# Kernel optimization log

Hardware: AMD Instinct MI355X
Metric: run time of the kernel (lower is better)

## Reference

```python
import jax, jax.numpy as jnp
import numpy as np

NUM_HEADS = 8
HEAD_CH = 32  # embed_channels // num_heads = 256 // 8
BN_EPS = 1e-3


def _conv(x, w, pad):
    return jax.lax.conv_general_dilated(
        x, w, window_strides=(1, 1), padding=[(pad, pad), (pad, pad)],
        dimension_numbers=('NCHW', 'OIHW', 'NCHW'))


def _bn(x, gamma, beta):
    # inference BN with running_mean=0, running_var=1 (fresh buffers)
    scale = gamma / jnp.sqrt(1.0 + BN_EPS)
    return x * scale[None, :, None, None] + beta[None, :, None, None]


def setup_inputs() -> dict:
    key = jax.random.key(0)
    ks = jax.random.split(key, 8)
    B, Cin, H, W = 16, 512, 40, 40
    N, Cg, E, Cout = 80, 512, 256, 512
    s = 0.05
    return {
        'x': jax.random.normal(ks[0], (B, Cin, H, W), jnp.float32),
        'guide': jax.random.normal(ks[1], (B, N, Cg), jnp.float32),
        'We': jax.random.normal(ks[2], (E, Cin, 1, 1), jnp.float32) * s,
        'gamma_e': jnp.ones((E,), jnp.float32),
        'beta_e': jnp.zeros((E,), jnp.float32),
        'Wg': jax.random.normal(ks[3], (E, Cg), jnp.float32) * s,
        'bg': jnp.zeros((E,), jnp.float32),
        'head_bias': jnp.zeros((NUM_HEADS,), jnp.float32),
        'Wp': jax.random.normal(ks[4], (Cout, Cin, 3, 3), jnp.float32) * s,
        'gamma_p': jnp.ones((Cout,), jnp.float32),
        'beta_p': jnp.zeros((Cout,), jnp.float32),
    }


def reference(x, guide, We, gamma_e, beta_e, Wg, bg, head_bias, Wp, gamma_p, beta_p):
    B, _, H, W = x.shape
    M, C = NUM_HEADS, HEAD_CH
    # guide_fc: [B, n, Cg] -> [B, n, M, C]
    g = (jnp.einsum('bnc,ec->bne', guide, Wg) + bg).reshape(B, -1, M, C)
    # embed_conv (1x1 + BN, no act): [B, M, C, H, W]
    e = _bn(_conv(x, We, 0), gamma_e, beta_e).reshape(B, M, C, H, W)
    # attention scores, max over guide tokens, scale, bias, sigmoid
    attn = jnp.einsum('bmchw,bnmc->bmhwn', e, g)
    attn = jnp.max(attn, axis=-1) / (C ** 0.5)
    attn = jax.nn.sigmoid(attn + head_bias[None, :, None, None])
    # project_conv (3x3 + BN, no act), gated per head
    p = _bn(_conv(x, Wp, 1), gamma_p, beta_p)
    p = p.reshape(B, M, -1, H, W) * attn[:, :, None, :, :]
    return p.reshape(B, -1, H, W)
```

## Files before the change

kernel.cpp:

```cpp
#include <hip/hip_runtime.h>
#include <hip/hip_bf16.h>
#include <stdint.h>

#define B_   16
#define CIN  512
#define HW   1600
#define E_   256
#define NTOK 80
#define CG   512
#define COUT 512
#define NHEAD 8
#define HCH  32
#define SP   (42*42)

typedef __attribute__((ext_vector_type(8))) short bf16x8;
typedef __attribute__((ext_vector_type(4))) float f32x4;
typedef unsigned short ushort_t;

__device__ __forceinline__ unsigned short f2bf(float f) {
  union { float f; unsigned int i; } v; v.f = f;
  unsigned int x = v.i;
  return (unsigned short)((x + 0x7FFFu + ((x >> 16) & 1u)) >> 16);
}

__global__ void k_prep_x(const float* __restrict__ x, unsigned short* __restrict__ xt) {
  __shared__ float tile[32][33];
  int hw0 = blockIdx.x * 32, ci0 = blockIdx.y * 32, b = blockIdx.z;
  int tx = threadIdx.x, ty = threadIdx.y;
  const float* xp = x + ((size_t)b * CIN + ci0) * HW + hw0;
#pragma unroll
  for (int j = 0; j < 4; j++) tile[ty + 8 * j][tx] = xp[(size_t)(ty + 8 * j) * HW + tx];
  __syncthreads();
  int ci = ci0 + tx;
#pragma unroll
  for (int j = 0; j < 4; j++) {
    int hw = hw0 + ty + 8 * j;
    int h = hw / 40, w = hw - h * 40;
    xt[((size_t)b * SP + (size_t)(h + 1) * 42 + (w + 1)) * CIN + ci] = f2bf(tile[tx][ty + 8 * j]);
  }
}

__global__ void k_prep_wp(const float* __restrict__ Wp, unsigned short* __restrict__ wpb2) {
  int idx = blockIdx.x * 256 + threadIdx.x;
  int co = idx >> 9, ci = idx & 511;
  const float* s = Wp + (size_t)idx * 9;
#pragma unroll
  for (int t = 0; t < 9; t++) wpb2[(size_t)co * (9 * CIN) + t * CIN + ci] = f2bf(s[t]);
}

__global__ void k_cast4(const float* __restrict__ in, unsigned short* __restrict__ out, int n4) {
  int i = blockIdx.x * 256 + threadIdx.x;
  if (i < n4) {
    float4 v = ((const float4*)in)[i];
    ushort4 o; o.x = f2bf(v.x); o.y = f2bf(v.y); o.z = f2bf(v.z); o.w = f2bf(v.w);
    ((ushort4*)out)[i] = o;
  }
}

template<int NTAPS, int EPI, int MT, int NT, int NB>
__launch_bounds__(256)
__global__ void k_conv(const unsigned short* __restrict__ Aw,
                       const unsigned short* __restrict__ Bsrc,
                       const float* __restrict__ gamma, const float* __restrict__ beta,
                       const float* __restrict__ attn, float* __restrict__ outp,
                       unsigned short* __restrict__ et, int Ncols) {
  constexpr int  RS    = NTAPS * CIN;
  constexpr int  NSTEP = NTAPS * (CIN / 32);
  constexpr bool BLIN  = (EPI == 2);
  __shared__ unsigned short L[3 * 8192];
  char* LB = (char*)L;
  int tid = threadIdx.x;

  int wg = blockIdx.x;
  if constexpr ((MT * NT * NB) % 8 == 0 && NB > 1) {
    constexpr int q = (MT * NT * NB) / 8;
    wg = (wg & 7) * q + (wg >> 3);
  }
  constexpr int PB = MT * NT;
  int b = wg / PB;
  int rem = wg - b * PB;
  int ntile = rem % NT;
  int mtile = rem / NT;
  int m0 = mtile * 128, n0 = ntile * 128;

  int lane = tid & 63, wid = tid >> 6;
  int wr = wid >> 1, wc = wid & 1;

  int mA = tid >> 2;
  int kq_log = (tid & 3) ^ ((tid >> 3) & 3);
  int kg = kq_log * 8;
  unsigned int lds0 = (unsigned int)tid * 16u, lds1 = (unsigned int)tid * 16u + 4096u;

  const unsigned short* pA = Aw + (size_t)(m0 + mA) * RS + kg;
  const unsigned short* pB0;
  const unsigned short* pB1;
  if constexpr (BLIN) {
    pB0 = Bsrc + (size_t)(n0 + mA) * CIN + kg;
    pB1 = Bsrc + (size_t)(n0 + mA + 64) * CIN + kg;
  } else {
    int hw_a = n0 + mA;      if (hw_a > HW - 1) hw_a = HW - 1;
    int hw_b = n0 + mA + 64; if (hw_b > HW - 1) hw_b = HW - 1;
    int ha = hw_a / 40, wa = hw_a - ha * 40;
    int hb = hw_b / 40, wb = hw_b - hb * 40;
    int sp_a = ha * 42 + wa + ((NTAPS == 1) ? 43 : 0);
    int sp_b = hb * 42 + wb + ((NTAPS == 1) ? 43 : 0);
    const unsigned short* xtb = Bsrc + (size_t)b * SP * CIN;
    pB0 = xtb + (size_t)sp_a * CIN + kg;
    pB1 = xtb + (size_t)sp_b * CIN + kg;
  }

  int scnt = 0;
  auto STG = [&](unsigned bo) {
    __builtin_amdgcn_global_load_lds((const __attribute__((address_space(1))) unsigned int*)pA,
        (__attribute__((address_space(3))) unsigned int*)(LB + bo + lds0), 16, 0, 0);
    __builtin_amdgcn_global_load_lds((const __attribute__((address_space(1))) unsigned int*)(pA + 64 * RS),
        (__attribute__((address_space(3))) unsigned int*)(LB + bo + lds1), 16, 0, 0);
    __builtin_amdgcn_global_load_lds((const __attribute__((address_space(1))) unsigned int*)pB0,
        (__attribute__((address_space(3))) unsigned int*)(LB + bo + 8192u + lds0), 16, 0, 0);
    __builtin_amdgcn_global_load_lds((const __attribute__((address_space(1))) unsigned int*)pB1,
        (__attribute__((address_space(3))) unsigned int*)(LB + bo + 8192u + lds1), 16, 0, 0);
    pA += 32; pB0 += 32; pB1 += 32;
    if constexpr (NTAPS > 1) {
      ++scnt;
      if ((scnt % 48) == 0) { pB0 += 19968; pB1 += 19968; }
    }
  };

  int frow = lane & 15;
  int kq16 = lane >> 4;
  int swz = (kq16 ^ ((frow >> 1) & 3)) << 4;
  int aoff[4], boff[4];
#pragma unroll
  for (int i = 0; i < 4; i++) {
    aoff[i] = (wr * 64 + i * 16 + frow) * 64 + swz;
    boff[i] = 8192 + (wc * 64 + i * 16 + frow) * 64 + swz;
  }

  f32x4 acc[4][4] = {};

  STG(0u); STG(16384u);
  unsigned r0 = 0u, r1 = 16384u, r2 = 32768u;
  for (int s = 0; s < NSTEP; ++s) {
    if (s + 1 < NSTEP) { asm volatile("s_waitcnt vmcnt(4)" ::: "memory"); }
    else               { asm volatile("s_waitcnt vmcnt(0)" ::: "memory"); }
    __builtin_amdgcn_s_barrier();
    __builtin_amdgcn_sched_barrier(0);
    if (s + 2 < NSTEP) STG(r2);
    const char* base = LB + r0;
    bf16x8 af[4], bfv[4];
#pragma unroll
    for (int i = 0; i < 4; i++) af[i] = *(const bf16x8*)(base + aoff[i]);
#pragma unroll
    for (int i = 0; i < 4; i++) bfv[i] = *(const bf16x8*)(base + boff[i]);
#pragma unroll
    for (int mi = 0; mi < 4; mi++)
#pragma unroll
      for (int ni = 0; ni < 4; ni++)
        acc[mi][ni] = __builtin_amdgcn_mfma_f32_16x16x32_bf16(af[mi], bfv[ni], acc[mi][ni], 0, 0, 0);
    unsigned t = r0; r0 = r1; r1 = r2; r2 = t;
  }

  const float BN_RSQ = 0.9995003746877732f;
  int colb = n0 + wc * 64 + frow;
  int rowb = m0 + wr * 64 + (lane >> 4) * 4;
  if constexpr (EPI == 1) {
    int head = (m0 + wr * 64) >> 6;
    const float* attn_b = attn + ((size_t)b * NHEAD + head) * HW;
    float* ob = outp + (size_t)b * COUT * HW;
#pragma unroll
    for (int mi = 0; mi < 4; mi++) {
      float sc[4], bt[4];
#pragma unroll
      for (int j = 0; j < 4; j++) {
        int co = rowb + mi * 16 + j;
        sc[j] = gamma[co] * BN_RSQ; bt[j] = beta[co];
      }
#pragma unroll
      for (int ni = 0; ni < 4; ni++) {
        int hw = colb + ni * 16;
        if (hw < Ncols) {
          float gate = attn_b[hw];
#pragma unroll
          for (int j = 0; j < 4; j++) {
            int co = rowb + mi * 16 + j;
            ob[(size_t)co * HW + hw] = (acc[mi][ni][j] * sc[j] + bt[j]) * gate;
          }
        }
      }
    }
  } else {
    unsigned short* etb = et + (EPI == 0 ? (size_t)b * HW * E_ : (size_t)0);
#pragma unroll
    for (int mi = 0; mi < 4; mi++) {
      float sc[4], bt[4];
#pragma unroll
      for (int j = 0; j < 4; j++) {
        int ech = rowb + mi * 16 + j;
        sc[j] = (EPI == 2) ? 1.0f : gamma[ech] * BN_RSQ;
        bt[j] = beta[ech];
      }
#pragma unroll
      for (int ni = 0; ni < 4; ni++) {
        int hw = colb + ni * 16;
        if (hw < Ncols) {
          ushort4 pk;
          pk.x = f2bf(acc[mi][ni][0] * sc[0] + bt[0]);
          pk.y = f2bf(acc[mi][ni][1] * sc[1] + bt[1]);
          pk.z = f2bf(acc[mi][ni][2] * sc[2] + bt[2]);
          pk.w = f2bf(acc[mi][ni][3] * sc[3] + bt[3]);
          *(ushort4*)(etb + (size_t)hw * E_ + (rowb + mi * 16)) = pk;
        }
      }
    }
  }
}

__global__ void k_attn_mfma(const unsigned short* __restrict__ et, const unsigned short* __restrict__ gbf,
                            const float* __restrict__ head_bias, float* __restrict__ attn) {
  __shared__ unsigned short gs[NTOK * HCH];
  int b = blockIdx.z, m = blockIdx.y;
  int tid = threadIdx.x, lane = tid & 63, wid = tid >> 6;
  for (int i = tid; i < NTOK * HCH / 8; i += 256) {
    int n = i >> 2, c = (i & 3) * 8;
    *(bf16x8*)&gs[n * HCH + c] = *(const bf16x8*)&gbf[((size_t)b * NTOK + n) * E_ + m * HCH + c];
  }
  __syncthreads();
  int col = lane & 15, kq = (lane >> 4) * 8;
  bf16x8 bfr[5];
#pragma unroll
  for (int ni = 0; ni < 5; ni++)
    bfr[ni] = *(const bf16x8*)&gs[(ni * 16 + col) * HCH + kq];

  int hw0 = blockIdx.x * 256 + wid * 64;
  bf16x8 afr[4];
#pragma unroll
  for (int mi = 0; mi < 4; mi++) {
    int hw = hw0 + mi * 16 + col; if (hw > HW - 1) hw = HW - 1;
    afr[mi] = *(const bf16x8*)&et[((size_t)b * HW + hw) * E_ + m * HCH + kq];
  }
  float hb = head_bias[m];
  float* attnp = attn + ((size_t)b * NHEAD + m) * HW;
#pragma unroll
  for (int mi = 0; mi < 4; mi++) {
    f32x4 d[5];
#pragma unroll
    for (int ni = 0; ni < 5; ni++) {
      f32x4 z = {0.f, 0.f, 0.f, 0.f};
      d[ni] = __builtin_amdgcn_mfma_f32_16x16x32_bf16(afr[mi], bfr[ni], z, 0, 0, 0);
    }
#pragma unroll
    for (int j = 0; j < 4; j++) {
      float v = fmaxf(fmaxf(fmaxf(d[0][j], d[1][j]), fmaxf(d[2][j], d[3][j])), d[4][j]);
      v = fmaxf(v, __shfl_xor(v, 1, 16));
      v = fmaxf(v, __shfl_xor(v, 2, 16));
      v = fmaxf(v, __shfl_xor(v, 4, 16));
      v = fmaxf(v, __shfl_xor(v, 8, 16));
      if (col == j) {
        int hwout = hw0 + mi * 16 + (lane >> 4) * 4 + j;
        if (hwout < HW)
          attnp[hwout] = 1.0f / (1.0f + __expf(-(v * 0.17677669529663687f + hb)));
      }
    }
  }
}

extern "C" void kernel_launch(void* const* d_in, const int* in_sizes, int n_in,
                              void* d_out, int out_size, void* d_ws, size_t ws_size,
                              hipStream_t stream) {
  const float* x         = (const float*)d_in[0];
  const float* guide     = (const float*)d_in[1];
  const float* We        = (const float*)d_in[2];
  const float* gamma_e   = (const float*)d_in[3];
  const float* beta_e    = (const float*)d_in[4];
  const float* Wg        = (const float*)d_in[5];
  const float* bg        = (const float*)d_in[6];
  const float* head_bias = (const float*)d_in[7];
  const float* Wp        = (const float*)d_in[8];
  const float* gamma_p   = (const float*)d_in[9];
  const float* beta_p    = (const float*)d_in[10];
  float* out = (float*)d_out;

  char* ws = (char*)d_ws;
  size_t off = 0;
  auto alloc = [&](size_t bytes) { char* p = ws + off; off += (bytes + 255) & ~(size_t)255; return p; };
  unsigned short* xt   = (unsigned short*)alloc((size_t)B_ * SP * CIN * 2);
  unsigned short* wpb2 = (unsigned short*)alloc((size_t)COUT * 9 * CIN * 2);
  unsigned short* web  = (unsigned short*)alloc((size_t)E_ * CIN * 2);
  unsigned short* wgb  = (unsigned short*)alloc((size_t)E_ * CG * 2);
  unsigned short* gub  = (unsigned short*)alloc((size_t)B_ * NTOK * CG * 2);
  unsigned short* gbf  = (unsigned short*)alloc((size_t)B_ * NTOK * E_ * 2);
  unsigned short* et   = (unsigned short*)alloc((size_t)B_ * HW * E_ * 2);
  float* attn          = (float*)alloc((size_t)B_ * NHEAD * HW * 4);

  hipMemsetAsync(xt, 0, (size_t)B_ * SP * CIN * 2, stream);
  k_prep_x<<<dim3(50, 16, B_), dim3(32, 8), 0, stream>>>(x, xt);
  k_prep_wp<<<dim3(1024), dim3(256), 0, stream>>>(Wp, wpb2);
  k_cast4<<<dim3(128), dim3(256), 0, stream>>>(We, web, E_ * CIN / 4);
  k_cast4<<<dim3(128), dim3(256), 0, stream>>>(Wg, wgb, E_ * CG / 4);
  k_cast4<<<dim3(640), dim3(256), 0, stream>>>(guide, gub, B_ * NTOK * CG / 4);
  k_conv<1, 2, 2, 10, 1><<<dim3(20), dim3(256), 0, stream>>>(wgb, gub, bg, bg, nullptr, nullptr, gbf, B_ * NTOK);
  k_conv<1, 0, 2, 13, B_><<<dim3(2 * 13 * B_), dim3(256), 0, stream>>>(web, xt, gamma_e, beta_e, nullptr, nullptr, et, HW);
  k_attn_mfma<<<dim3(7, NHEAD, B_), dim3(256), 0, stream>>>(et, gbf, head_bias, attn);
  k_conv<9, 1, 4, 13, B_><<<dim3(4 * 13 * B_), dim3(256), 0, stream>>>(wpb2, xt, gamma_p, beta_p, attn, out, nullptr, HW);
}
```

Measured before the change: 327.1 us.

## Enlarge GEMM tiles to 256x128 and flatten batch into column dimension

```diff
diff --git a/kernel.cpp b/kernel.cpp
--- a/kernel.cpp
+++ b/kernel.cpp
@@ -15,7 +15,6 @@
 
 typedef __attribute__((ext_vector_type(8))) short bf16x8;
 typedef __attribute__((ext_vector_type(4))) float f32x4;
-typedef unsigned short ushort_t;
 
 __device__ __forceinline__ unsigned short f2bf(float f) {
   union { float f; unsigned int i; } v; v.f = f;
@@ -48,77 +47,74 @@
   for (int t = 0; t < 9; t++) wpb2[(size_t)co * (9 * CIN) + t * CIN + ci] = f2bf(s[t]);
 }
 
-__global__ void k_cast4(const float* __restrict__ in, unsigned short* __restrict__ out, int n4) {
+__global__ void k_cast_all(const float* __restrict__ We, unsigned short* __restrict__ web,
+                           const float* __restrict__ Wg, unsigned short* __restrict__ wgb,
+                           const float* __restrict__ gu, unsigned short* __restrict__ gub) {
   int i = blockIdx.x * 256 + threadIdx.x;
-  if (i < n4) {
-    float4 v = ((const float4*)in)[i];
-    ushort4 o; o.x = f2bf(v.x); o.y = f2bf(v.y); o.z = f2bf(v.z); o.w = f2bf(v.w);
-    ((ushort4*)out)[i] = o;
-  }
-}
-
-template<int NTAPS, int EPI, int MT, int NT, int NB>
-__launch_bounds__(256)
+  const float* src; unsigned short* dst; int j;
+  if (i < 32768)       { src = We; dst = web; j = i; }
+  else if (i < 65536)  { src = Wg; dst = wgb; j = i - 32768; }
+  else                 { src = gu; dst = gub; j = i - 65536; }
+  float4 v = ((const float4*)src)[j];
+  ushort4 o; o.x = f2bf(v.x); o.y = f2bf(v.y); o.z = f2bf(v.z); o.w = f2bf(v.w);
+  ((ushort4*)dst)[j] = o;
+}
+
+template<int NTAPS, int EPI, int MT, int NT, int SWZ>
+__launch_bounds__(256, 2)
 __global__ void k_conv(const unsigned short* __restrict__ Aw,
                        const unsigned short* __restrict__ Bsrc,
                        const float* __restrict__ gamma, const float* __restrict__ beta,
                        const float* __restrict__ attn, float* __restrict__ outp,
-                       unsigned short* __restrict__ et, int Ncols) {
+                       unsigned short* __restrict__ et) {
   constexpr int  RS    = NTAPS * CIN;
   constexpr int  NSTEP = NTAPS * (CIN / 32);
   constexpr bool BLIN  = (EPI == 2);
-  __shared__ unsigned short L[3 * 8192];
+  __shared__ unsigned short L[3 * 12288];
   char* LB = (char*)L;
   int tid = threadIdx.x;
 
   int wg = blockIdx.x;
-  if constexpr ((MT * NT * NB) % 8 == 0 && NB > 1) {
-    constexpr int q = (MT * NT * NB) / 8;
+  if constexpr (SWZ) {
+    constexpr int q = MT * NT / 8;
     wg = (wg & 7) * q + (wg >> 3);
   }
-  constexpr int PB = MT * NT;
-  int b = wg / PB;
-  int rem = wg - b * PB;
-  int ntile = rem % NT;
-  int mtile = rem / NT;
-  int m0 = mtile * 128, n0 = ntile * 128;
+  int mtile = wg / NT, ntile = wg % NT;
+  int m0 = mtile * 256, n0 = ntile * 128;
 
   int lane = tid & 63, wid = tid >> 6;
   int wr = wid >> 1, wc = wid & 1;
 
-  int mA = tid >> 2;
-  int kq_log = (tid & 3) ^ ((tid >> 3) & 3);
-  int kg = kq_log * 8;
-  unsigned int lds0 = (unsigned int)tid * 16u, lds1 = (unsigned int)tid * 16u + 4096u;
-
-  const unsigned short* pA = Aw + (size_t)(m0 + mA) * RS + kg;
+  int rA = tid >> 2;
+  int kq = ((tid & 3) ^ ((tid >> 3) & 3)) * 8;
+  const unsigned short* pA = Aw + (size_t)(m0 + rA) * RS + kq;
   const unsigned short* pB0;
   const unsigned short* pB1;
   if constexpr (BLIN) {
-    pB0 = Bsrc + (size_t)(n0 + mA) * CIN + kg;
-    pB1 = Bsrc + (size_t)(n0 + mA + 64) * CIN + kg;
+    pB0 = Bsrc + (size_t)(n0 + rA) * CIN + kq;
+    pB1 = pB0 + (size_t)64 * CIN;
   } else {
-    int hw_a = n0 + mA;      if (hw_a > HW - 1) hw_a = HW - 1;
-    int hw_b = n0 + mA + 64; if (hw_b > HW - 1) hw_b = HW - 1;
-    int ha = hw_a / 40, wa = hw_a - ha * 40;
-    int hb = hw_b / 40, wb = hw_b - hb * 40;
-    int sp_a = ha * 42 + wa + ((NTAPS == 1) ? 43 : 0);
-    int sp_b = hb * 42 + wb + ((NTAPS == 1) ? 43 : 0);
-    const unsigned short* xtb = Bsrc + (size_t)b * SP * CIN;
-    pB0 = xtb + (size_t)sp_a * CIN + kg;
-    pB1 = xtb + (size_t)sp_b * CIN + kg;
+    int c0 = n0 + rA, c1 = c0 + 64;
+    int b0 = c0 / 1600, hw0 = c0 - b0 * 1600;
+    int b1 = c1 / 1600, hw1 = c1 - b1 * 1600;
+    int h0 = hw0 / 40, w0 = hw0 - h0 * 40;
+    int h1 = hw1 / 40, w1 = hw1 - h1 * 40;
+    constexpr int ctr = (NTAPS == 1) ? 43 : 0;
+    pB0 = Bsrc + ((size_t)b0 * SP + h0 * 42 + w0 + ctr) * CIN + kq;
+    pB1 = Bsrc + ((size_t)b1 * SP + h1 * 42 + w1 + ctr) * CIN + kq;
   }
 
   int scnt = 0;
   auto STG = [&](unsigned bo) {
-    __builtin_amdgcn_global_load_lds((const __attribute__((address_space(1))) unsigned int*)pA,
-        (__attribute__((address_space(3))) unsigned int*)(LB + bo + lds0), 16, 0, 0);
-    __builtin_amdgcn_global_load_lds((const __attribute__((address_space(1))) unsigned int*)(pA + 64 * RS),
-        (__attribute__((address_space(3))) unsigned int*)(LB + bo + lds1), 16, 0, 0);
-    __builtin_amdgcn_global_load_lds((const __attribute__((address_space(1))) unsigned int*)pB0,
-        (__attribute__((address_space(3))) unsigned int*)(LB + bo + 8192u + lds0), 16, 0, 0);
-    __builtin_amdgcn_global_load_lds((const __attribute__((address_space(1))) unsigned int*)pB1,
-        (__attribute__((address_space(3))) unsigned int*)(LB + bo + 8192u + lds1), 16, 0, 0);
+#define GL(src, dst) __builtin_amdgcn_global_load_lds((const __attribute__((address_space(1))) unsigned int*)(src), \
+        (__attribute__((address_space(3))) unsigned int*)(dst), 16, 0, 0)
+    GL(pA,            LB + bo +      0u + tid * 16u);
+    GL(pA +  64 * RS, LB + bo +  4096u + tid * 16u);
+    GL(pA + 128 * RS, LB + bo +  8192u + tid * 16u);
+    GL(pA + 192 * RS, LB + bo + 12288u + tid * 16u);
+    GL(pB0,           LB + bo + 16384u + tid * 16u);
+    GL(pB1,           LB + bo + 20480u + tid * 16u);
+#undef GL
     pA += 32; pB0 += 32; pB1 += 32;
     if constexpr (NTAPS > 1) {
       ++scnt;
@@ -127,48 +123,45 @@
   };
 
   int frow = lane & 15;
-  int kq16 = lane >> 4;
-  int swz = (kq16 ^ ((frow >> 1) & 3)) << 4;
-  int aoff[4], boff[4];
-#pragma unroll
-  for (int i = 0; i < 4; i++) {
-    aoff[i] = (wr * 64 + i * 16 + frow) * 64 + swz;
-    boff[i] = 8192 + (wc * 64 + i * 16 + frow) * 64 + swz;
-  }
-
-  f32x4 acc[4][4] = {};
-
-  STG(0u); STG(16384u);
-  unsigned r0 = 0u, r1 = 16384u, r2 = 32768u;
+  int swz = ((lane >> 4) ^ ((frow >> 1) & 3)) << 4;
+  int aoff[8], boff[4];
+#pragma unroll
+  for (int i = 0; i < 8; i++) aoff[i] = (wr * 128 + i * 16 + frow) * 64 + swz;
+#pragma unroll
+  for (int i = 0; i < 4; i++) boff[i] = 16384 + (wc * 64 + i * 16 + frow) * 64 + swz;
+
+  f32x4 acc[8][4] = {};
+
+  STG(0u); STG(24576u);
+  unsigned r0 = 0u, r1 = 24576u, r2 = 49152u;
   for (int s = 0; s < NSTEP; ++s) {
-    if (s + 1 < NSTEP) { asm volatile("s_waitcnt vmcnt(4)" ::: "memory"); }
+    if (s + 1 < NSTEP) { asm volatile("s_waitcnt vmcnt(6)" ::: "memory"); }
     else               { asm volatile("s_waitcnt vmcnt(0)" ::: "memory"); }
     __builtin_amdgcn_s_barrier();
     __builtin_amdgcn_sched_barrier(0);
     if (s + 2 < NSTEP) STG(r2);
     const char* base = LB + r0;
-    bf16x8 af[4], bfv[4];
-#pragma unroll
-    for (int i = 0; i < 4; i++) af[i] = *(const bf16x8*)(base + aoff[i]);
-#pragma unroll
-    for (int i = 0; i < 4; i++) bfv[i] = *(const bf16x8*)(base + boff[i]);
-#pragma unroll
-    for (int mi = 0; mi < 4; mi++)
+    bf16x8 af[8], bv[4];
+#pragma unroll
+    for (int i = 0; i < 8; i++) af[i] = *(const bf16x8*)(base + aoff[i]);
+#pragma unroll
+    for (int i = 0; i < 4; i++) bv[i] = *(const bf16x8*)(base + boff[i]);
+#pragma unroll
+    for (int mi = 0; mi < 8; mi++)
 #pragma unroll
       for (int ni = 0; ni < 4; ni++)
-        acc[mi][ni] = __builtin_amdgcn_mfma_f32_16x16x32_bf16(af[mi], bfv[ni], acc[mi][ni], 0, 0, 0);
+        acc[mi][ni] = __builtin_amdgcn_mfma_f32_16x16x32_bf16(af[mi], bv[ni], acc[mi][ni], 0, 0, 0);
     unsigned t = r0; r0 = r1; r1 = r2; r2 = t;
   }
 
   const float BN_RSQ = 0.9995003746877732f;
   int colb = n0 + wc * 64 + frow;
-  int rowb = m0 + wr * 64 + (lane >> 4) * 4;
+  int rowb = m0 + wr * 128 + (lane >> 4) * 4;
   if constexpr (EPI == 1) {
-    int head = (m0 + wr * 64) >> 6;
-    const float* attn_b = attn + ((size_t)b * NHEAD + head) * HW;
-    float* ob = outp + (size_t)b * COUT * HW;
-#pragma unroll
-    for (int mi = 0; mi < 4; mi++) {
+    float* ob = outp;
+#pragma unroll
+    for (int mi = 0; mi < 8; mi++) {
+      int head = (m0 + wr * 128 + mi * 16) >> 6;
       float sc[4], bt[4];
 #pragma unroll
       for (int j = 0; j < 4; j++) {
@@ -177,21 +170,19 @@
       }
 #pragma unroll
       for (int ni = 0; ni < 4; ni++) {
-        int hw = colb + ni * 16;
-        if (hw < Ncols) {
-          float gate = attn_b[hw];
-#pragma unroll
-          for (int j = 0; j < 4; j++) {
-            int co = rowb + mi * 16 + j;
-            ob[(size_t)co * HW + hw] = (acc[mi][ni][j] * sc[j] + bt[j]) * gate;
-          }
+        int col = colb + ni * 16;
+        int b = col / 1600, hw = col - b * 1600;
+        float gate = attn[((size_t)b * NHEAD + head) * HW + hw];
+#pragma unroll
+        for (int j = 0; j < 4; j++) {
+          int co = rowb + mi * 16 + j;
+          ob[((size_t)b * COUT + co) * HW + hw] = (acc[mi][ni][j] * sc[j] + bt[j]) * gate;
         }
       }
     }
   } else {
-    unsigned short* etb = et + (EPI == 0 ? (size_t)b * HW * E_ : (size_t)0);
-#pragma unroll
-    for (int mi = 0; mi < 4; mi++) {
+#pragma unroll
+    for (int mi = 0; mi < 8; mi++) {
       float sc[4], bt[4];
 #pragma unroll
       for (int j = 0; j < 4; j++) {
@@ -201,15 +192,20 @@
       }
 #pragma unroll
       for (int ni = 0; ni < 4; ni++) {
-        int hw = colb + ni * 16;
-        if (hw < Ncols) {
-          ushort4 pk;
-          pk.x = f2bf(acc[mi][ni][0] * sc[0] + bt[0]);
-          pk.y = f2bf(acc[mi][ni][1] * sc[1] + bt[1]);
-          pk.z = f2bf(acc[mi][ni][2] * sc[2] + bt[2]);
-          pk.w = f2bf(acc[mi][ni][3] * sc[3] + bt[3]);
-          *(ushort4*)(etb + (size_t)hw * E_ + (rowb + mi * 16)) = pk;
+        int col = colb + ni * 16;
+        size_t rowbase;
+        if constexpr (EPI == 2) {
+          rowbase = (size_t)col * E_;
+        } else {
+          int b = col / 1600, hw = col - b * 1600;
+          rowbase = ((size_t)b * HW + hw) * E_;
         }
+        ushort4 pk;
+        pk.x = f2bf(acc[mi][ni][0] * sc[0] + bt[0]);
+        pk.y = f2bf(acc[mi][ni][1] * sc[1] + bt[1]);
+        pk.z = f2bf(acc[mi][ni][2] * sc[2] + bt[2]);
+        pk.w = f2bf(acc[mi][ni][3] * sc[3] + bt[3]);
+        *(ushort4*)(et + rowbase + (rowb + mi * 16)) = pk;
       }
     }
   }
@@ -295,11 +291,9 @@
   hipMemsetAsync(xt, 0, (size_t)B_ * SP * CIN * 2, stream);
   k_prep_x<<<dim3(50, 16, B_), dim3(32, 8), 0, stream>>>(x, xt);
   k_prep_wp<<<dim3(1024), dim3(256), 0, stream>>>(Wp, wpb2);
-  k_cast4<<<dim3(128), dim3(256), 0, stream>>>(We, web, E_ * CIN / 4);
-  k_cast4<<<dim3(128), dim3(256), 0, stream>>>(Wg, wgb, E_ * CG / 4);
-  k_cast4<<<dim3(640), dim3(256), 0, stream>>>(guide, gub, B_ * NTOK * CG / 4);
-  k_conv<1, 2, 2, 10, 1><<<dim3(20), dim3(256), 0, stream>>>(wgb, gub, bg, bg, nullptr, nullptr, gbf, B_ * NTOK);
-  k_conv<1, 0, 2, 13, B_><<<dim3(2 * 13 * B_), dim3(256), 0, stream>>>(web, xt, gamma_e, beta_e, nullptr, nullptr, et, HW);
+  k_cast_all<<<dim3(896), dim3(256), 0, stream>>>(We, web, Wg, wgb, guide, gub);
+  k_conv<1, 2, 1, 10, 0><<<dim3(10), dim3(256), 0, stream>>>(wgb, gub, bg, bg, nullptr, nullptr, gbf);
+  k_conv<1, 0, 1, 200, 1><<<dim3(200), dim3(256), 0, stream>>>(web, xt, gamma_e, beta_e, nullptr, nullptr, et);
   k_attn_mfma<<<dim3(7, NHEAD, B_), dim3(256), 0, stream>>>(et, gbf, head_bias, attn);
-  k_conv<9, 1, 4, 13, B_><<<dim3(4 * 13 * B_), dim3(256), 0, stream>>>(wpb2, xt, gamma_p, beta_p, attn, out, nullptr, HW);
-}
+  k_conv<9, 1, 2, 200, 1><<<dim3(400), dim3(256), 0, stream>>>(wpb2, xt, gamma_p, beta_p, attn, out, nullptr);
+}
```

Measured after the change: 309.5 us. -5.4%, faster.
